# Kernel tuning notes

Measured on AMD Instinct MI355X. Metric: run time of the kernel, lower is better.

## Reference

```python
import jax, jax.numpy as jnp
import numpy as np

H = 16          # num_heads
W = 256         # attention_window
D_MODEL = 1024
D_FF = 4096
EPS = 1e-5


def _layernorm(x, g, b):
    mu = jnp.mean(x, axis=-1, keepdims=True)
    var = jnp.mean(jnp.square(x - mu), axis=-1, keepdims=True)
    return (x - mu) * jax.lax.rsqrt(var + EPS) * g + b


def _sliding_attn(q, k, v, w):
    # q,k,v: [B,H,S,d]; each query attends to keys in [i-w, i+w]
    B, Hh, S, d = q.shape
    nc = S // w
    qc = q.reshape(B, Hh, nc, w, d)
    kp = jnp.pad(k, ((0, 0), (0, 0), (w, w), (0, 0)))
    vp = jnp.pad(v, ((0, 0), (0, 0), (w, w), (0, 0)))
    # gather 3w keys per chunk (prev w, current w, next w)
    idx = (jnp.arange(nc) * w)[:, None] + jnp.arange(3 * w)[None, :]  # [nc, 3w]
    kc = kp[:, :, idx, :]  # [B,H,nc,3w,d]
    vc = vp[:, :, idx, :]
    scores = jnp.einsum('bhcqd,bhckd->bhcqk', qc, kc)  # [B,H,nc,w,3w]
    q_pos = jnp.arange(nc)[:, None, None] * w + jnp.arange(w)[None, :, None]
    k_pos = jnp.arange(nc)[:, None, None] * w - w + jnp.arange(3 * w)[None, None, :]
    rel = k_pos - q_pos
    valid = (jnp.abs(rel) <= w) & (k_pos >= 0) & (k_pos < S)  # [nc,w,3w]
    scores = jnp.where(valid[None, None], scores, jnp.float32(-1e9))
    p = jax.nn.softmax(scores, axis=-1)
    out = jnp.einsum('bhcqk,bhckd->bhcqd', p, vc)
    return out.reshape(B, Hh, S, d)


def setup_inputs() -> dict:
    key = jax.random.key(0)
    ks = jax.random.split(key, 8)
    B, S = 2, 4096
    src = jax.random.normal(ks[0], (B, S, D_MODEL), dtype=jnp.float32)
    ln1_g = jnp.ones((D_MODEL,), jnp.float32)
    ln1_b = jnp.zeros((D_MODEL,), jnp.float32)
    ln2_g = jnp.ones((D_MODEL,), jnp.float32)
    ln2_b = jnp.zeros((D_MODEL,), jnp.float32)
    W1 = jax.random.normal(ks[1], (D_MODEL, D_FF), jnp.float32) * 0.02
    b1 = jnp.zeros((D_FF,), jnp.float32)
    W2 = jax.random.normal(ks[2], (D_FF, D_MODEL), jnp.float32) * 0.02
    b2 = jnp.zeros((D_MODEL,), jnp.float32)
    return {"src": src, "ln1_g": ln1_g, "ln1_b": ln1_b, "ln2_g": ln2_g,
            "ln2_b": ln2_b, "W1": W1, "b1": b1, "W2": W2, "b2": b2}


def reference(src, ln1_g, ln1_b, ln2_g, ln2_b, W1, b1, W2, b2):
    B, S, _ = src.shape
    d_head = D_MODEL // H
    qkv = src.reshape(B, S, H, d_head).transpose(0, 2, 1, 3)  # [B,H,S,d]
    attn = _sliding_attn(qkv, qkv, qkv, W)
    attn = attn.transpose(0, 2, 1, 3).reshape(B, S, D_MODEL)
    x = _layernorm(src + attn, ln1_g, ln1_b)
    ff = jnp.maximum(x @ W1 + b1, 0.0) @ W2 + b2
    return _layernorm(x + ff, ln2_g, ln2_b)
```

## Files before the change

### kernel.cpp

```cpp
#include <hip/hip_runtime.h>

typedef __bf16 bf16x8 __attribute__((ext_vector_type(8)));
typedef __bf16 bf16x4 __attribute__((ext_vector_type(4)));
typedef float f32x4 __attribute__((ext_vector_type(4)));

#define MFMA16(a, b, c) __builtin_amdgcn_mfma_f32_16x16x32_bf16((a), (b), (c), 0, 0, 0)

__device__ __forceinline__ void gload_lds16(const void* g, void* l) {
  __builtin_amdgcn_global_load_lds(
      (const __attribute__((address_space(1))) unsigned int*)g,
      (__attribute__((address_space(3))) unsigned int*)l, 16, 0, 0);
}

__global__ __launch_bounds__(256, 2) void attn_kernel(const float* __restrict__ src,
                                                      __bf16* __restrict__ attn_out) {
  const int bid = blockIdx.x;
  const int half = bid & 1;
  const int c = (bid >> 1) & 15;
  const int h = (bid >> 5) & 15;
  const int b = bid >> 9;
  const int tid = threadIdx.x;
  const int w = tid >> 6;
  const int lane = tid & 63;
  const int lg = lane >> 4;
  const int l16 = lane & 15;
  const size_t b4096 = (size_t)b * 4096;

  __shared__ __bf16 Ks[2][64][72];
  __shared__ __bf16 Vt[2][64][72];

  const int q0 = c * 256 + half * 128 + w * 32;
  const float LOG2E = 1.44269504f;

  bf16x8 qf[2][2];
#pragma unroll
  for (int qfi = 0; qfi < 2; ++qfi)
#pragma unroll
    for (int ks = 0; ks < 2; ++ks) {
      const int row = q0 + qfi * 16 + l16;
      const int d0 = ks * 32 + lg * 8;
      const float* p = src + (b4096 + row) * 1024 + h * 64 + d0;
      bf16x8 v;
#pragma unroll
      for (int j = 0; j < 8; ++j) v[j] = (__bf16)(p[j] * LOG2E);
      qf[qfi][ks] = v;
    }

  int krow[4];
#pragma unroll
  for (int kf = 0; kf < 4; ++kf)
    krow[kf] = ((kf >> 1) << 5) + ((l16 >> 2) << 3) + ((kf & 1) << 2) + (l16 & 3);

  const f32x4 z4 = {0.f, 0.f, 0.f, 0.f};
  float m_run[2], l_run[2];
  f32x4 o[2][4];
#pragma unroll
  for (int qfi = 0; qfi < 2; ++qfi) {
    m_run[qfi] = -6.0e8f;
    l_run[qfi] = 0.f;
#pragma unroll
    for (int df = 0; df < 4; ++df) o[qfi][df] = z4;
  }

  const int stage_key = tid >> 2;
  const int d0a = (tid & 3) * 16;
  const int vcolA = stage_key ^ d0a;
  const int vcolB = stage_key ^ (d0a + 8);

  int kpos = c * 256 - 256 + stage_key;
  float4 g4[4];
  {
    const int rc = min(max(kpos, 0), 4095);
    const float* p = src + (b4096 + rc) * 1024 + h * 64 + d0a;
#pragma unroll
    for (int i = 0; i < 4; ++i) g4[i] = *(const float4*)(p + i * 4);
  }

  for (int kt = 0; kt < 12; ++kt) {
    const int kbase = c * 256 - 256 + kt * 64;
    const int cur = kt & 1;
    bf16x8 kvA, kvB;
    const bool inb = ((unsigned)kpos < 4096u);
    kvA[0] = (__bf16)(inb ? g4[0].x : 0.f); kvA[1] = (__bf16)(inb ? g4[0].y : 0.f);
    kvA[2] = (__bf16)(inb ? g4[0].z : 0.f); kvA[3] = (__bf16)(inb ? g4[0].w : 0.f);
    kvA[4] = (__bf16)(inb ? g4[1].x : 0.f); kvA[5] = (__bf16)(inb ? g4[1].y : 0.f);
    kvA[6] = (__bf16)(inb ? g4[1].z : 0.f); kvA[7] = (__bf16)(inb ? g4[1].w : 0.f);
    kvB[0] = (__bf16)(inb ? g4[2].x : 0.f); kvB[1] = (__bf16)(inb ? g4[2].y : 0.f);
    kvB[2] = (__bf16)(inb ? g4[2].z : 0.f); kvB[3] = (__bf16)(inb ? g4[2].w : 0.f);
    kvB[4] = (__bf16)(inb ? g4[3].x : 0.f); kvB[5] = (__bf16)(inb ? g4[3].y : 0.f);
    kvB[6] = (__bf16)(inb ? g4[3].z : 0.f); kvB[7] = (__bf16)(inb ? g4[3].w : 0.f);

    *(bf16x8*)&Ks[cur][stage_key][d0a] = kvA;
    *(bf16x8*)&Ks[cur][stage_key][d0a + 8] = kvB;
#pragma unroll
    for (int j = 0; j < 8; ++j) Vt[cur][d0a + j][vcolA] = kvA[j];
#pragma unroll
    for (int j = 0; j < 8; ++j) Vt[cur][d0a + 8 + j][vcolB] = kvB[j];
    asm volatile("s_waitcnt lgkmcnt(0)" ::: "memory");
    __builtin_amdgcn_s_barrier();
    __builtin_amdgcn_sched_barrier(0);

    kpos += 64;
    if (kt < 11) {
      const int rc = min(max(kpos, 0), 4095);
      const float* p = src + (b4096 + rc) * 1024 + h * 64 + d0a;
#pragma unroll
      for (int i = 0; i < 4; ++i) g4[i] = *(const float4*)(p + i * 4);
    }

    const bool skip = (kbase + 63 < 0) | (kbase >= 4096) |
                      (kbase + 63 < q0 - 256) | (kbase > q0 + 31 + 256);
    if (skip) continue;

    f32x4 s[4][2];
#pragma unroll
    for (int kf = 0; kf < 4; ++kf)
#pragma unroll
      for (int qfi = 0; qfi < 2; ++qfi) s[kf][qfi] = z4;

#pragma unroll
    for (int ks = 0; ks < 2; ++ks) {
      bf16x8 ka[4];
#pragma unroll
      for (int kf = 0; kf < 4; ++kf)
        ka[kf] = *(const bf16x8*)&Ks[cur][krow[kf]][ks * 32 + lg * 8];
#pragma unroll
      for (int kf = 0; kf < 4; ++kf)
#pragma unroll
        for (int qfi = 0; qfi < 2; ++qfi)
          s[kf][qfi] = MFMA16(ka[kf], qf[qfi][ks], s[kf][qfi]);
    }

    const bool needmask = (kbase < 0) | (kbase > 4032) |
                          (kbase < q0 - 225) | (kbase > q0 + 193);
    if (needmask) {
#pragma unroll
      for (int qfi = 0; qfi < 2; ++qfi) {
        const int qp = q0 + qfi * 16 + l16;
#pragma unroll
        for (int kf = 0; kf < 4; ++kf) {
          const int kb0 = kbase + ((kf >> 1) << 5) + 8 * lg + ((kf & 1) << 2);
#pragma unroll
          for (int reg = 0; reg < 4; ++reg) {
            const int kp = kb0 + reg;
            const int rel = kp - qp;
            if (rel > 256 || rel < -256 || kp < 0 || kp >= 4096)
              s[kf][qfi][reg] = -1e9f;
          }
        }
      }
    }

    bf16x4 pb[4][2];
#pragma unroll
    for (int qfi = 0; qfi < 2; ++qfi) {
      float tm = s[0][qfi][0];
#pragma unroll
      for (int kf = 0; kf < 4; ++kf)
#pragma unroll
        for (int reg = 0; reg < 4; ++reg) tm = fmaxf(tm, s[kf][qfi][reg]);
      tm = fmaxf(tm, __shfl_xor(tm, 16, 64));
      tm = fmaxf(tm, __shfl_xor(tm, 32, 64));

      const bool nomax = __all(tm <= m_run[qfi] + 8.f);
      float scl = 1.f;
      if (!nomax) {
        const float mn = fmaxf(m_run[qfi], tm);
        scl = exp2f(m_run[qfi] - mn);
        m_run[qfi] = mn;
#pragma unroll
        for (int df = 0; df < 4; ++df)
#pragma unroll
          for (int reg = 0; reg < 4; ++reg) o[qfi][df][reg] *= scl;
      }
      const float mn = m_run[qfi];

      float rs = 0.f;
#pragma unroll
      for (int kf = 0; kf < 4; ++kf) {
        bf16x4 pv;
#pragma unroll
        for (int reg = 0; reg < 4; ++reg) {
          const float p = exp2f(s[kf][qfi][reg] - mn);
          rs += p;
          pv[reg] = (__bf16)p;
        }
        pb[kf][qfi] = pv;
      }
      rs += __shfl_xor(rs, 16, 64);
      rs += __shfl_xor(rs, 32, 64);
      l_run[qfi] = l_run[qfi] * scl + rs;
    }

#pragma unroll
    for (int ks2 = 0; ks2 < 2; ++ks2) {
      bf16x8 av[4];
#pragma unroll
      for (int df = 0; df < 4; ++df) {
        const int d = df * 16 + l16;
        const int blk = (ks2 * 4 + lg) ^ (d >> 3);
        av[df] = *(const bf16x8*)&Vt[cur][d][blk * 8];
      }
#pragma unroll
      for (int qfi = 0; qfi < 2; ++qfi) {
        const bf16x8 bq = __builtin_shufflevector(pb[2 * ks2][qfi], pb[2 * ks2 + 1][qfi],
                                                  0, 1, 2, 3, 4, 5, 6, 7);
#pragma unroll
        for (int df = 0; df < 4; ++df)
          o[qfi][df] = MFMA16(av[df], bq, o[qfi][df]);
      }
    }
  }

#pragma unroll
  for (int qfi = 0; qfi < 2; ++qfi) {
    const float inv = 1.0f / l_run[qfi];
    const int qp = q0 + qfi * 16 + l16;
    __bf16* dst = attn_out + (b4096 + qp) * 1024 + h * 64 + lg * 4;
#pragma unroll
    for (int df = 0; df < 4; ++df) {
      bf16x4 y;
      y[0] = (__bf16)(o[qfi][df][0] * inv);
      y[1] = (__bf16)(o[qfi][df][1] * inv);
      y[2] = (__bf16)(o[qfi][df][2] * inv);
      y[3] = (__bf16)(o[qfi][df][3] * inv);
      *(bf16x4*)&dst[df * 16] = y;
    }
  }
}

template <int MODE>
__global__ __launch_bounds__(512, 2) void gemm8p(const __bf16* __restrict__ A,
                                                 const __bf16* __restrict__ Bt,
                                                 const float* __restrict__ bias,
                                                 __bf16* __restrict__ out,
                                                 size_t ksplit_stride,
                                                 int M, int N, int Kstride, int Klen) {
  __shared__ char smem[131072];
  const int tid = threadIdx.x;
  const int w = tid >> 6;
  const int lane = tid & 63;
  const int lg = lane >> 4;
  const int l16 = lane & 15;
  const int wr = w >> 2;
  const int wc = w & 3;

  const int nbn = N >> 8;
  const int x = ((int)blockIdx.x & 7) * ((int)gridDim.x >> 3) + ((int)blockIdx.x >> 3);
  const long bm = (long)(x / nbn) * 256;
  const long bn = (long)(x % nbn) * 256;
  const long koff = (long)blockIdx.y * Klen;
  out += (size_t)blockIdx.y * ksplit_stride;

  const f32x4 z4 = {0.f, 0.f, 0.f, 0.f};
  f32x4 acc[8][4];
#pragma unroll
  for (int i = 0; i < 8; ++i)
#pragma unroll
    for (int j = 0; j < 4; ++j) acc[i][j] = z4;

  const int srow = tid >> 2;
  const int g0 = (tid & 3) ^ ((tid >> 3) & 3);
  const __bf16* Ag = A + (size_t)(bm + srow) * Kstride + koff + g0 * 8;
  const __bf16* Bg = Bt + (size_t)(bn + srow) * Kstride + koff + g0 * 8;

  auto stage = [&](int kt) {
    char* da = smem + ((kt & 3) << 15) + (w << 10);
    const size_t o = (size_t)kt * 32;
    gload_lds16(Ag + o, da);
    gload_lds16(Ag + o + (size_t)128 * Kstride, da + 8192);
    gload_lds16(Bg + o, da + 16384);
    gload_lds16(Bg + o + (size_t)128 * Kstride, da + 16384 + 8192);
  };

  const int lslot = (lg ^ ((l16 >> 1) & 3)) << 4;
  const char* pA = smem + (wr * 128 + l16) * 64 + lslot;
  const char* pB = smem + 16384 + (wc * 64 + l16) * 64 + lslot;
  auto rdA = [&](int buf, int rf) {
    return *(const bf16x8*)(pA + (buf << 15) + rf * 1024);
  };
  auto rdB = [&](int buf, int cf) {
    return *(const bf16x8*)(pB + (buf << 15) + cf * 1024);
  };

  const int NT = Klen >> 5;

  stage(0); stage(1); stage(2); stage(3);
  asm volatile("s_waitcnt vmcnt(12)" ::: "memory");
  __builtin_amdgcn_s_barrier();
  __builtin_amdgcn_sched_barrier(0);

  for (int t = 0; t < NT; ++t) {
    const int buf = t & 3;
    if (t > 0 && t + 3 < NT) stage(t + 3);

    bf16x8 af[8], bf[4];
#pragma unroll
    for (int rf = 0; rf < 8; ++rf) af[rf] = rdA(buf, rf);
#pragma unroll
    for (int cf = 0; cf < 4; ++cf) bf[cf] = rdB(buf, cf);

    __builtin_amdgcn_s_setprio(1);
#pragma unroll
    for (int rf = 0; rf < 8; ++rf)
#pragma unroll
      for (int cf = 0; cf < 4; ++cf)
        acc[rf][cf] = MFMA16(af[rf], bf[cf], acc[rf][cf]);
    __builtin_amdgcn_s_setprio(0);

    const int nfly = min(2, NT - 2 - t);
    if (nfly >= 2)      asm volatile("s_waitcnt vmcnt(8)" ::: "memory");
    else if (nfly == 1) asm volatile("s_waitcnt vmcnt(4)" ::: "memory");
    else                asm volatile("s_waitcnt vmcnt(0)" ::: "memory");
    __builtin_amdgcn_s_barrier();
    __builtin_amdgcn_sched_barrier(0);
  }

  float bv[4];
  if (MODE == 0) {
#pragma unroll
    for (int cf = 0; cf < 4; ++cf) bv[cf] = bias[bn + wc * 64 + cf * 16 + l16];
  }
#pragma unroll
  for (int rf = 0; rf < 8; ++rf)
#pragma unroll
    for (int reg = 0; reg < 4; ++reg) {
      const long row = bm + wr * 128 + rf * 16 + lg * 4 + reg;
#pragma unroll
      for (int cf = 0; cf < 4; ++cf) {
        const long col = bn + wc * 64 + cf * 16 + l16;
        if (MODE == 0) {
          out[row * N + col] = (__bf16)fmaxf(acc[rf][cf][reg] + bv[cf], 0.f);
        } else {
          out[row * N + col] = (__bf16)acc[rf][cf][reg];
        }
      }
    }
}

__global__ __launch_bounds__(256) void transpose_cvt(const float* __restrict__ in,
                                                     __bf16* __restrict__ out,
                                                     int R, int C) {
  __shared__ float tile[64][65];
  const long r0 = (long)blockIdx.y * 64;
  const long c0 = (long)blockIdx.x * 64;
  const int t = threadIdx.x;
  const int tr = t >> 6;
  const int tc = t & 63;
#pragma unroll
  for (int i = 0; i < 16; ++i) {
    const int r = tr * 16 + i;
    tile[r][tc] = in[(r0 + r) * C + c0 + tc];
  }
  __syncthreads();
#pragma unroll
  for (int i = 0; i < 16; ++i) {
    const int cc = tr * 16 + i;
    out[(c0 + cc) * (long)R + r0 + tc] = (__bf16)tile[tc][cc];
  }
}

__global__ __launch_bounds__(256) void ln1_kernel(const float* __restrict__ src,
                                                  const __bf16* __restrict__ attn,
                                                  const float* __restrict__ g,
                                                  const float* __restrict__ bta,
                                                  __bf16* __restrict__ xb) {
  const long r = blockIdx.x;
  const int t = threadIdx.x;
  const float4 a = *(const float4*)&src[r * 1024 + t * 4];
  const bf16x4 cc = *(const bf16x4*)&attn[r * 1024 + t * 4];
  float v[4] = {a.x + (float)cc[0], a.y + (float)cc[1],
                a.z + (float)cc[2], a.w + (float)cc[3]};
  float s = v[0] + v[1] + v[2] + v[3];
  float s2 = v[0] * v[0] + v[1] * v[1] + v[2] * v[2] + v[3] * v[3];
#pragma unroll
  for (int off = 32; off >= 1; off >>= 1) {
    s += __shfl_xor(s, off, 64);
    s2 += __shfl_xor(s2, off, 64);
  }
  __shared__ float red[8];
  if ((t & 63) == 0) { red[t >> 6] = s; red[(t >> 6) + 4] = s2; }
  __syncthreads();
  s = red[0] + red[1] + red[2] + red[3];
  s2 = red[4] + red[5] + red[6] + red[7];
  const float mu = s * (1.f / 1024.f);
  const float var = s2 * (1.f / 1024.f) - mu * mu;
  const float rstd = rsqrtf(var + 1e-5f);
  const float4 gv = *(const float4*)&g[t * 4];
  const float4 bv = *(const float4*)&bta[t * 4];
  bf16x4 y;
  y[0] = (__bf16)((v[0] - mu) * rstd * gv.x + bv.x);
  y[1] = (__bf16)((v[1] - mu) * rstd * gv.y + bv.y);
  y[2] = (__bf16)((v[2] - mu) * rstd * gv.z + bv.z);
  y[3] = (__bf16)((v[3] - mu) * rstd * gv.w + bv.w);
  *(bf16x4*)&xb[r * 1024 + t * 4] = y;
}

__global__ __launch_bounds__(256) void ln2_kernel(const __bf16* __restrict__ xb,
                                                  const __bf16* __restrict__ f0,
                                                  const __bf16* __restrict__ f1,
                                                  const float* __restrict__ b2,
                                                  const float* __restrict__ g,
                                                  const float* __restrict__ bta,
                                                  float* __restrict__ out) {
  const long r = blockIdx.x;
  const int t = threadIdx.x;
  const bf16x4 xv = *(const bf16x4*)&xb[r * 1024 + t * 4];
  const bf16x4 f0v = *(const bf16x4*)&f0[r * 1024 + t * 4];
  const bf16x4 f1v = *(const bf16x4*)&f1[r * 1024 + t * 4];
  const float4 b2v = *(const float4*)&b2[t * 4];
  float v[4];
#pragma unroll
  for (int i = 0; i < 4; ++i)
    v[i] = (float)xv[i] + (float)f0v[i] + (float)f1v[i] +
           ((const float*)&b2v)[i];
  float s = v[0] + v[1] + v[2] + v[3];
  float s2 = v[0] * v[0] + v[1] * v[1] + v[2] * v[2] + v[3] * v[3];
#pragma unroll
  for (int off = 32; off >= 1; off >>= 1) {
    s += __shfl_xor(s, off, 64);
    s2 += __shfl_xor(s2, off, 64);
  }
  __shared__ float red[8];
  if ((t & 63) == 0) { red[t >> 6] = s; red[(t >> 6) + 4] = s2; }
  __syncthreads();
  s = red[0] + red[1] + red[2] + red[3];
  s2 = red[4] + red[5] + red[6] + red[7];
  const float mu = s * (1.f / 1024.f);
  const float var = s2 * (1.f / 1024.f) - mu * mu;
  const float rstd = rsqrtf(var + 1e-5f);
  const float4 gv = *(const float4*)&g[t * 4];
  const float4 bv = *(const float4*)&bta[t * 4];
  float4 y;
  y.x = (v[0] - mu) * rstd * gv.x + bv.x;
  y.y = (v[1] - mu) * rstd * gv.y + bv.y;
  y.z = (v[2] - mu) * rstd * gv.z + bv.z;
  y.w = (v[3] - mu) * rstd * gv.w + bv.w;
  *(float4*)&out[r * 1024 + t * 4] = y;
}

extern "C" void kernel_launch(void* const* d_in, const int* in_sizes, int n_in,
                              void* d_out, int out_size, void* d_ws, size_t ws_size,
                              hipStream_t stream) {
  const float* src = (const float*)d_in[0];
  const float* ln1_g = (const float*)d_in[1];
  const float* ln1_b = (const float*)d_in[2];
  const float* ln2_g = (const float*)d_in[3];
  const float* ln2_b = (const float*)d_in[4];
  const float* W1 = (const float*)d_in[5];
  const float* b1 = (const float*)d_in[6];
  const float* W2 = (const float*)d_in[7];
  const float* b2 = (const float*)d_in[8];
  float* out = (float*)d_out;
  char* ws = (char*)d_ws;

  const size_t MB = 1048576;
  __bf16* xb = (__bf16*)ws;
  __bf16* attn_b = (__bf16*)(ws + 16 * MB);
  __bf16* ffb = attn_b;
  __bf16* ff1b = (__bf16*)(ws + 32 * MB);
  __bf16* w1t = (__bf16*)(ws + 48 * MB);
  __bf16* w2t = (__bf16*)(ws + 56 * MB);
  __bf16* hbuf = (__bf16*)(ws + 64 * MB);

  int Mc = 8192;
  while (Mc > 512 && 64 * MB + (size_t)Mc * 8192 > ws_size) Mc >>= 1;

  transpose_cvt<<<dim3(4096 / 64, 1024 / 64), 256, 0, stream>>>(W1, w1t, 1024, 4096);
  transpose_cvt<<<dim3(1024 / 64, 4096 / 64), 256, 0, stream>>>(W2, w2t, 4096, 1024);
  attn_kernel<<<1024, 256, 0, stream>>>(src, attn_b);
  ln1_kernel<<<8192, 256, 0, stream>>>(src, attn_b, ln1_g, ln1_b, xb);
  for (int m0 = 0; m0 < 8192; m0 += Mc) {
    gemm8p<0><<<dim3((Mc / 256) * (4096 / 256), 1), 512, 0, stream>>>(
        xb + (size_t)m0 * 1024, w1t, b1, hbuf, 0, Mc, 4096, 1024, 1024);
    gemm8p<1><<<dim3((Mc / 256) * (1024 / 256), 2), 512, 0, stream>>>(
        hbuf, w2t, nullptr, ffb + (size_t)m0 * 1024, (size_t)8192 * 1024,
        Mc, 1024, 4096, 2048);
  }
  ln2_kernel<<<8192, 256, 0, stream>>>(xb, ffb, ff1b, b2, ln2_g, ln2_b, out);
}
```

Measured before the change: 239.6 us.

## Restructure GEMM pipeline to double-buffered 64-wide K tiles and raise attention occupancy

The GEMM main loop moves from a 4-slot ring of 32-wide K stages to a 2-slot double buffer of 64-wide K tiles, each split into two halves. Each half's loads are issued right after its fragments are read into registers, with a barrier after every half-step. This changes how prefetch depth and barriers line up, aiming for better overlap of global-to-LDS loads with MFMA work. The attention kernel's launch bounds also go from 2 to 4 blocks per CU, which caps its register use and may cause spills.

```diff
diff --git a/kernel.cpp b/kernel.cpp
--- a/kernel.cpp
+++ b/kernel.cpp
@@ -12,7 +12,7 @@
       (__attribute__((address_space(3))) unsigned int*)l, 16, 0, 0);
 }
 
-__global__ __launch_bounds__(256, 2) void attn_kernel(const float* __restrict__ src,
+__global__ __launch_bounds__(256, 4) void attn_kernel(const float* __restrict__ src,
                                                       __bf16* __restrict__ attn_out) {
   const int bid = blockIdx.x;
   const int half = bid & 1;
@@ -264,42 +264,43 @@
   const __bf16* Ag = A + (size_t)(bm + srow) * Kstride + koff + g0 * 8;
   const __bf16* Bg = Bt + (size_t)(bn + srow) * Kstride + koff + g0 * 8;
 
-  auto stage = [&](int kt) {
-    char* da = smem + ((kt & 3) << 15) + (w << 10);
-    const size_t o = (size_t)kt * 32;
-    gload_lds16(Ag + o, da);
-    gload_lds16(Ag + o + (size_t)128 * Kstride, da + 8192);
-    gload_lds16(Bg + o, da + 16384);
-    gload_lds16(Bg + o + (size_t)128 * Kstride, da + 16384 + 8192);
+  auto stage = [&](int kt, int osel, int isB, int khalf) {
+    const __bf16* src = (isB ? Bg : Ag) + (size_t)kt * 64 + khalf * 32;
+    char* dst = smem + (isB ? 65536 : 0) + osel * 32768 + khalf * 16384 + (w << 10);
+    gload_lds16(src, dst);
+    gload_lds16(src + (size_t)128 * Kstride, dst + 8192);
   };
 
   const int lslot = (lg ^ ((l16 >> 1) & 3)) << 4;
   const char* pA = smem + (wr * 128 + l16) * 64 + lslot;
-  const char* pB = smem + 16384 + (wc * 64 + l16) * 64 + lslot;
-  auto rdA = [&](int buf, int rf) {
-    return *(const bf16x8*)(pA + (buf << 15) + rf * 1024);
+  const char* pB = smem + 65536 + (wc * 64 + l16) * 64 + lslot;
+  auto rdA = [&](int sel, int rf, int ks) {
+    return *(const bf16x8*)(pA + sel * 32768 + ks * 16384 + rf * 1024);
   };
-  auto rdB = [&](int buf, int cf) {
-    return *(const bf16x8*)(pB + (buf << 15) + cf * 1024);
+  auto rdB = [&](int sel, int cf, int ks) {
+    return *(const bf16x8*)(pB + sel * 32768 + ks * 16384 + cf * 1024);
   };
 
-  const int NT = Klen >> 5;
-
-  stage(0); stage(1); stage(2); stage(3);
-  asm volatile("s_waitcnt vmcnt(12)" ::: "memory");
+  const int NT = Klen >> 6;
+
+  stage(0, 0, 0, 0);
+  stage(0, 0, 1, 0);
+  stage(0, 0, 0, 1);
+  stage(0, 0, 1, 1);
+  asm volatile("s_waitcnt vmcnt(4)" ::: "memory");
   __builtin_amdgcn_s_barrier();
   __builtin_amdgcn_sched_barrier(0);
 
   for (int t = 0; t < NT; ++t) {
-    const int buf = t & 3;
-    if (t > 0 && t + 3 < NT) stage(t + 3);
-
+    const int sel = t & 1, osel = sel ^ 1;
+    const bool st = (t + 1) < NT;
     bf16x8 af[8], bf[4];
-#pragma unroll
-    for (int rf = 0; rf < 8; ++rf) af[rf] = rdA(buf, rf);
-#pragma unroll
-    for (int cf = 0; cf < 4; ++cf) bf[cf] = rdB(buf, cf);
-
+
+#pragma unroll
+    for (int rf = 0; rf < 8; ++rf) af[rf] = rdA(sel, rf, 0);
+#pragma unroll
+    for (int cf = 0; cf < 4; ++cf) bf[cf] = rdB(sel, cf, 0);
+    if (st) { stage(t + 1, osel, 0, 0); stage(t + 1, osel, 1, 0); }
     __builtin_amdgcn_s_setprio(1);
 #pragma unroll
     for (int rf = 0; rf < 8; ++rf)
@@ -307,11 +308,24 @@
       for (int cf = 0; cf < 4; ++cf)
         acc[rf][cf] = MFMA16(af[rf], bf[cf], acc[rf][cf]);
     __builtin_amdgcn_s_setprio(0);
-
-    const int nfly = min(2, NT - 2 - t);
-    if (nfly >= 2)      asm volatile("s_waitcnt vmcnt(8)" ::: "memory");
-    else if (nfly == 1) asm volatile("s_waitcnt vmcnt(4)" ::: "memory");
-    else                asm volatile("s_waitcnt vmcnt(0)" ::: "memory");
+    if (st) asm volatile("s_waitcnt vmcnt(4)" ::: "memory");
+    else    asm volatile("s_waitcnt vmcnt(0)" ::: "memory");
+    __builtin_amdgcn_s_barrier();
+    __builtin_amdgcn_sched_barrier(0);
+
+#pragma unroll
+    for (int rf = 0; rf < 8; ++rf) af[rf] = rdA(sel, rf, 1);
+#pragma unroll
+    for (int cf = 0; cf < 4; ++cf) bf[cf] = rdB(sel, cf, 1);
+    if (st) { stage(t + 1, osel, 0, 1); stage(t + 1, osel, 1, 1); }
+    __builtin_amdgcn_s_setprio(1);
+#pragma unroll
+    for (int rf = 0; rf < 8; ++rf)
+#pragma unroll
+      for (int cf = 0; cf < 4; ++cf)
+        acc[rf][cf] = MFMA16(af[rf], bf[cf], acc[rf][cf]);
+    __builtin_amdgcn_s_setprio(0);
+    if (st) asm volatile("s_waitcnt vmcnt(4)" ::: "memory");
     __builtin_amdgcn_s_barrier();
     __builtin_amdgcn_sched_barrier(0);
   }
```

Result: slower. 274.9 us (+14.7%).
